# Kernel optimization log

Hardware: AMD Instinct MI355X
Metric: run time of the kernel (lower is better)

## Reference

```python
import jax, jax.numpy as jnp
import numpy as np
from jax import lax

LRELU_SLOPE = 0.2
GAIN = 2.0 ** 0.5
EPS = 1e-8


def setup_inputs() -> dict:
    key = jax.random.key(0)
    ks = jax.random.split(key, 8)
    B, NDW, CIN, COUT, H, W = 4, 512, 16, 16, 1024, 1024
    return {
        "w": jax.random.normal(ks[0], (B, NDW), jnp.float32),
        "x": jax.random.normal(ks[1], (B, CIN, H, W), jnp.float32),
        "noise": jax.random.normal(ks[2], (B, 1, H, W), jnp.float32),
        "fc_weight": jax.random.normal(ks[3], (CIN, NDW), jnp.float32),
        "fc_bias": jnp.ones((CIN,), jnp.float32),
        "conv_weight": jax.random.normal(ks[4], (COUT, CIN, 3, 3), jnp.float32),
        "conv_bias": jax.random.normal(ks[5], (COUT,), jnp.float32),
        "scale_noise": jnp.float32(0.1),
    }


def reference(w, x, noise, fc_weight, fc_bias, conv_weight, conv_bias, scale_noise):
    NDW = fc_weight.shape[1]
    COUT, CIN, KH, KW = conv_weight.shape
    # equal_lr scaling (FC): weight * n_dim_in**-0.5
    s = w @ (fc_weight.T * (NDW ** -0.5)) + fc_bias  # [B, CIN] style per input channel
    # equal_lr scaling (Conv): weight * (in_channels * k^2)**-0.5
    wc = conv_weight * ((CIN * KH * KW) ** -0.5)  # [COUT, CIN, 3, 3]
    # demodulation coefficient: d[b,o] = 1/sqrt(sum_{i,kh,kw} (s[b,i]*wc[o,i,kh,kw])^2 + eps)
    w2 = (wc ** 2).sum(axis=(2, 3))  # [COUT, CIN]
    d = lax.rsqrt((s ** 2) @ w2.T + EPS)  # [B, COUT]
    # modulate input instead of materializing per-sample weights (mathematically identical)
    xm = x * s[:, :, None, None]
    y = lax.conv_general_dilated(
        xm, wc, window_strides=(1, 1), padding=((1, 1), (1, 1)),
        dimension_numbers=("NCHW", "OIHW", "NCHW"))
    y = y * d[:, :, None, None] + conv_bias[None, :, None, None]
    y = y + scale_noise * noise  # broadcast noise over channels
    y = GAIN * jnp.where(y >= 0, y, LRELU_SLOPE * y)
    return (w, y)
```

## Files before the change

### kernel.cpp

```cpp
#include <hip/hip_runtime.h>

#define H_ 1024
#define W_ 1024
#define B_ 4
#define CIN 16
#define COUT 16
#define TH 8
#define TW 64
#define LDS_COLS 66
#define LDS_ROWS 10

#define LRELU 0.2f
#define GAIN_ 1.4142135623730951f
#define EPS_ 1e-8f

typedef __attribute__((ext_vector_type(8))) short bf16x8;
typedef __attribute__((ext_vector_type(4))) float f32x4;

static __device__ __forceinline__ unsigned short f32_to_bf16(float f) {
    unsigned int u = __float_as_uint(f);
    unsigned int r = u + 0x7FFF + ((u >> 16) & 1);
    return (unsigned short)(r >> 16);
}

__global__ __launch_bounds__(256) void k_setup1(
    const float* __restrict__ w, const float* __restrict__ fcw,
    const float* __restrict__ fcb, float* __restrict__ s_out,
    float* __restrict__ w_copy_out)
{
    __shared__ float part[256];
    const int tid = threadIdx.x;
    const int bi = tid >> 2;
    const int q  = tid & 3;
    const int b = bi >> 4, i = bi & 15;
    const float* wr = w + b * 512 + q * 128;
    const float* fr = fcw + i * 512 + q * 128;
    float acc = 0.f;
    #pragma unroll 8
    for (int k = 0; k < 128; ++k) acc += wr[k] * fr[k];
    part[tid] = acc;
    __syncthreads();
    if (tid < 64) {
        float v = part[tid*4] + part[tid*4+1] + part[tid*4+2] + part[tid*4+3];
        s_out[tid] = v * 0.04419417382415922f  + fcb[tid & 15];
    }
    for (int e = tid; e < B_ * 512; e += 256) w_copy_out[e] = w[e];
}

__global__ __launch_bounds__(256) void k_setup2(
    const float* __restrict__ s_in, const float* __restrict__ convw,
    unsigned short* __restrict__ afrag)
{
    const int b = blockIdx.x;
    const int tid = threadIdx.x;
    __shared__ float s_sh[16];
    __shared__ float d_sh[16];
    __shared__ float wc_sh[COUT * CIN * 9];
    __shared__ float part[256];

    if (tid < 16) s_sh[tid] = s_in[b * 16 + tid];
    for (int e = tid; e < COUT * CIN * 9; e += 256)
        wc_sh[e] = convw[e] * (1.0f / 12.0f);
    __syncthreads();

    const int o = tid >> 4, i = tid & 15;
    const float si = s_sh[i];
    float acc = 0.f;
    #pragma unroll
    for (int tap = 0; tap < 9; ++tap) {
        float v = wc_sh[(o * 16 + i) * 9 + tap] * si;
        acc += v * v;
    }
    part[tid] = acc;
    __syncthreads();
    if (tid < 16) {
        float sum = EPS_;
        #pragma unroll
        for (int j = 0; j < 16; ++j) sum += part[tid * 16 + j];
        d_sh[tid] = rsqrtf(sum);
    }
    __syncthreads();

    for (int e = tid; e < 5 * 64 * 8; e += 256) {
        int t = e >> 9;
        int lane = (e >> 3) & 63;
        int j = e & 7;
        int oo = lane & 15, g = lane >> 4;
        int ii = (g & 1) * 8 + j;
        int tap = 2 * t + (g >> 1);
        float v = 0.f;
        if (tap < 9) v = wc_sh[(oo * 16 + ii) * 9 + tap] * s_sh[ii] * d_sh[oo];
        afrag[(size_t)b * (5 * 64 * 8) + e] = f32_to_bf16(v);
    }
}

__global__ __launch_bounds__(256) void k_conv(
    const float* __restrict__ x, const float* __restrict__ noise,
    const float* __restrict__ conv_bias, const float* __restrict__ sn_ptr,
    const unsigned short* __restrict__ afrag, float* __restrict__ y)
{
    __shared__ unsigned short tile[2][LDS_ROWS][LDS_COLS][8];

    const int tid = threadIdx.x;
    const int bt = blockIdx.z;
    const int h0 = blockIdx.y * TH;
    const int w0 = blockIdx.x * TW;
    const float sn = sn_ptr[0];
    const float* xb = x + (size_t)bt * CIN * H_ * W_;

    if (tid < 160) {
        const int row = tid >> 4;
        const int cg  = tid & 15;
        const int gh  = h0 - 1 + row;
        const bool okr = (gh >= 0) && (gh < H_);
        #pragma unroll
        for (int h = 0; h < 2; ++h) {
            float4 v[8];
            #pragma unroll
            for (int c = 0; c < 8; ++c) {
                v[c] = make_float4(0.f, 0.f, 0.f, 0.f);
                if (okr)
                    v[c] = *reinterpret_cast<const float4*>(
                        xb + ((size_t)(8 * h + c) * H_ + gh) * W_ + (w0 + 4 * cg));
            }
            #pragma unroll
            for (int px = 0; px < 4; ++px) {
                bf16x8 pk;
                pk[0] = (short)f32_to_bf16(px == 0 ? v[0].x : px == 1 ? v[0].y : px == 2 ? v[0].z : v[0].w);
                pk[1] = (short)f32_to_bf16(px == 0 ? v[1].x : px == 1 ? v[1].y : px == 2 ? v[1].z : v[1].w);
                pk[2] = (short)f32_to_bf16(px == 0 ? v[2].x : px == 1 ? v[2].y : px == 2 ? v[2].z : v[2].w);
                pk[3] = (short)f32_to_bf16(px == 0 ? v[3].x : px == 1 ? v[3].y : px == 2 ? v[3].z : v[3].w);
                pk[4] = (short)f32_to_bf16(px == 0 ? v[4].x : px == 1 ? v[4].y : px == 2 ? v[4].z : v[4].w);
                pk[5] = (short)f32_to_bf16(px == 0 ? v[5].x : px == 1 ? v[5].y : px == 2 ? v[5].z : v[5].w);
                pk[6] = (short)f32_to_bf16(px == 0 ? v[6].x : px == 1 ? v[6].y : px == 2 ? v[6].z : v[6].w);
                pk[7] = (short)f32_to_bf16(px == 0 ? v[7].x : px == 1 ? v[7].y : px == 2 ? v[7].z : v[7].w);
                *reinterpret_cast<bf16x8*>(&tile[h][row][1 + 4 * cg + px][0]) = pk;
            }
        }
    } else if (tid < 180) {
        const int u    = tid - 160;
        const int row  = u >> 1;
        const int side = u & 1;
        const int col  = side * (LDS_COLS - 1);
        const int gh   = h0 - 1 + row;
        const int gw   = w0 - 1 + col;
        const bool ok  = (gh >= 0) && (gh < H_) && (gw >= 0) && (gw < W_);
        #pragma unroll
        for (int h = 0; h < 2; ++h) {
            bf16x8 pk;
            #pragma unroll
            for (int c = 0; c < 8; ++c) {
                float v = ok ? xb[((size_t)(8 * h + c) * H_ + gh) * W_ + gw] : 0.f;
                pk[c] = (short)f32_to_bf16(v);
            }
            *reinterpret_cast<bf16x8*>(&tile[h][row][col][0]) = pk;
        }
    }

    const int lane  = tid & 63;
    const int wid   = tid >> 6;
    const int p     = lane & 15;
    const int g     = lane >> 4;
    const int ghalf = g >> 1;
    const int chalf = g & 1;

    bf16x8 a[5];
    {
        const bf16x8* ap =
            reinterpret_cast<const bf16x8*>(afrag + (size_t)bt * 5 * 64 * 8);
        #pragma unroll
        for (int t = 0; t < 5; ++t) a[t] = ap[t * 64 + lane];
    }
    float bias_j[4];
    #pragma unroll
    for (int j = 0; j < 4; ++j) bias_j[j] = conv_bias[g * 4 + j];

    int lroff[5], lcoff[5];
    #pragma unroll
    for (int t = 0; t < 5; ++t) {
        int tap = 2 * t + ghalf;
        if (tap > 8) tap = 8;
        lroff[t] = tap / 3;
        lcoff[t] = tap % 3;
    }

    __syncthreads();

    float* yb = y + (size_t)bt * COUT * H_ * W_;
    const float* nb = noise + (size_t)bt * H_ * W_;

    #pragma unroll
    for (int rr = 0; rr < 2; ++rr) {
        const int oh = wid * 2 + rr;
        #pragma unroll
        for (int gc = 0; gc < 4; ++gc) {
            const int ow = gc * 16;
            f32x4 acc = {0.f, 0.f, 0.f, 0.f};
            #pragma unroll
            for (int t = 0; t < 5; ++t) {
                const bf16x8 bv = *reinterpret_cast<const bf16x8*>(
                    &tile[chalf][oh + lroff[t]][ow + p + lcoff[t]][0]);
                acc = __builtin_amdgcn_mfma_f32_16x16x32_bf16(a[t], bv, acc, 0, 0, 0);
            }
            const int gh = h0 + oh;
            const int gw = w0 + ow + p;
            const float noi = nb[(size_t)gh * W_ + gw] * sn;
            #pragma unroll
            for (int j = 0; j < 4; ++j) {
                float v = acc[j] + bias_j[j] + noi;
                v = (v >= 0.f) ? v : (LRELU * v);
                yb[((size_t)(g * 4 + j) * H_ + gh) * W_ + gw] = v * GAIN_;
            }
        }
    }
}

extern "C" void kernel_launch(void* const* d_in, const int* in_sizes, int n_in,
                              void* d_out, int out_size, void* d_ws, size_t ws_size,
                              hipStream_t stream)
{
    const float* w     = (const float*)d_in[0];
    const float* x     = (const float*)d_in[1];
    const float* noise = (const float*)d_in[2];
    const float* fcw   = (const float*)d_in[3];
    const float* fcb   = (const float*)d_in[4];
    const float* convw = (const float*)d_in[5];
    const float* convb = (const float*)d_in[6];
    const float* sn    = (const float*)d_in[7];

    float* out = (float*)d_out;
    float* ws_s = (float*)d_ws;
    unsigned short* ws_afrag = (unsigned short*)((char*)d_ws + 256);

    k_setup1<<<1, 256, 0, stream>>>(w, fcw, fcb, ws_s, out);
    k_setup2<<<B_, 256, 0, stream>>>(ws_s, convw, ws_afrag);
    dim3 grid(W_ / TW, H_ / TH, B_);
    k_conv<<<grid, 256, 0, stream>>>(x, noise, convb, sn, ws_afrag, out + 2048);
}
```

Measured before the change: 181.3 us.

## Loop each block over eight row tiles with double-buffered LDS staging

Each block now walks NT=8 consecutive 8-row tiles of a narrower 32-column strip. The global loads for the next tile are issued into registers before computing the current one and written to a second LDS buffer afterwards, so memory latency overlaps MFMA work. The padded LDS layout with a per-half column offset is meant to reduce bank conflicts, and the launch bound requests higher occupancy. In exchange the grid is much smaller and the narrower tile raises the halo overhead per column, so the vertical halo reloads per tile stay.

```diff
diff --git a/kernel.cpp b/kernel.cpp
--- a/kernel.cpp
+++ b/kernel.cpp
@@ -6,9 +6,11 @@
 #define CIN 16
 #define COUT 16
 #define TH 8
-#define TW 64
-#define LDS_COLS 66
-#define LDS_ROWS 10
+#define TW 32
+#define NT 8
+#define ROWS 10
+#define COLS 34
+#define COLS_P 36
 
 #define LRELU 0.2f
 #define GAIN_ 1.4142135623730951f
@@ -94,68 +96,21 @@
     }
 }
 
-__global__ __launch_bounds__(256) void k_conv(
+__global__ __launch_bounds__(256, 4) void k_conv(
     const float* __restrict__ x, const float* __restrict__ noise,
     const float* __restrict__ conv_bias, const float* __restrict__ sn_ptr,
     const unsigned short* __restrict__ afrag, float* __restrict__ y)
 {
-    __shared__ unsigned short tile[2][LDS_ROWS][LDS_COLS][8];
+    __shared__ unsigned short tile[2 * 2 * ROWS * COLS_P * 8];
 
     const int tid = threadIdx.x;
     const int bt = blockIdx.z;
-    const int h0 = blockIdx.y * TH;
+    const int h0 = blockIdx.y * (TH * NT);
     const int w0 = blockIdx.x * TW;
     const float sn = sn_ptr[0];
     const float* xb = x + (size_t)bt * CIN * H_ * W_;
-
-    if (tid < 160) {
-        const int row = tid >> 4;
-        const int cg  = tid & 15;
-        const int gh  = h0 - 1 + row;
-        const bool okr = (gh >= 0) && (gh < H_);
-        #pragma unroll
-        for (int h = 0; h < 2; ++h) {
-            float4 v[8];
-            #pragma unroll
-            for (int c = 0; c < 8; ++c) {
-                v[c] = make_float4(0.f, 0.f, 0.f, 0.f);
-                if (okr)
-                    v[c] = *reinterpret_cast<const float4*>(
-                        xb + ((size_t)(8 * h + c) * H_ + gh) * W_ + (w0 + 4 * cg));
-            }
-            #pragma unroll
-            for (int px = 0; px < 4; ++px) {
-                bf16x8 pk;
-                pk[0] = (short)f32_to_bf16(px == 0 ? v[0].x : px == 1 ? v[0].y : px == 2 ? v[0].z : v[0].w);
-                pk[1] = (short)f32_to_bf16(px == 0 ? v[1].x : px == 1 ? v[1].y : px == 2 ? v[1].z : v[1].w);
-                pk[2] = (short)f32_to_bf16(px == 0 ? v[2].x : px == 1 ? v[2].y : px == 2 ? v[2].z : v[2].w);
-                pk[3] = (short)f32_to_bf16(px == 0 ? v[3].x : px == 1 ? v[3].y : px == 2 ? v[3].z : v[3].w);
-                pk[4] = (short)f32_to_bf16(px == 0 ? v[4].x : px == 1 ? v[4].y : px == 2 ? v[4].z : v[4].w);
-                pk[5] = (short)f32_to_bf16(px == 0 ? v[5].x : px == 1 ? v[5].y : px == 2 ? v[5].z : v[5].w);
-                pk[6] = (short)f32_to_bf16(px == 0 ? v[6].x : px == 1 ? v[6].y : px == 2 ? v[6].z : v[6].w);
-                pk[7] = (short)f32_to_bf16(px == 0 ? v[7].x : px == 1 ? v[7].y : px == 2 ? v[7].z : v[7].w);
-                *reinterpret_cast<bf16x8*>(&tile[h][row][1 + 4 * cg + px][0]) = pk;
-            }
-        }
-    } else if (tid < 180) {
-        const int u    = tid - 160;
-        const int row  = u >> 1;
-        const int side = u & 1;
-        const int col  = side * (LDS_COLS - 1);
-        const int gh   = h0 - 1 + row;
-        const int gw   = w0 - 1 + col;
-        const bool ok  = (gh >= 0) && (gh < H_) && (gw >= 0) && (gw < W_);
-        #pragma unroll
-        for (int h = 0; h < 2; ++h) {
-            bf16x8 pk;
-            #pragma unroll
-            for (int c = 0; c < 8; ++c) {
-                float v = ok ? xb[((size_t)(8 * h + c) * H_ + gh) * W_ + gw] : 0.f;
-                pk[c] = (short)f32_to_bf16(v);
-            }
-            *reinterpret_cast<bf16x8*>(&tile[h][row][col][0]) = pk;
-        }
-    }
+    float* yb = y + (size_t)bt * COUT * H_ * W_;
+    const float* nb = noise + (size_t)bt * H_ * W_;
 
     const int lane  = tid & 63;
     const int wid   = tid >> 6;
@@ -164,10 +119,65 @@
     const int ghalf = g >> 1;
     const int chalf = g & 1;
 
+    const bool is_int  = (tid < 160);
+    const bool is_edge = (tid >= 160) && (tid < 200);
+    const int s_row = is_int ? (tid >> 4) : ((tid - 160) >> 2);
+    const int s_sub = tid & 15;
+    const int s_hh  = is_int ? (s_sub >> 3) : ((tid - 160) & 1);
+    const int s_cg  = s_sub & 7;
+    const int s_side = ((tid - 160) >> 1) & 1;
+
+    auto toff = [&](int buf, int half, int row, int col) -> int {
+        return (((buf * 2 + half) * ROWS + row) * COLS_P + col + 2 * half) * 8;
+    };
+
+    float4 v[8];
+    float  ev[8];
+
+    auto stage_load = [&](int t) {
+        const int gh0 = h0 + TH * t - 1;
+        if (is_int) {
+            const int gh = gh0 + s_row;
+            const bool ok = (gh >= 0) && (gh < H_);
+            const float* base = xb + ((size_t)(8 * s_hh) * H_ + gh) * W_ + (w0 + 4 * s_cg);
+            #pragma unroll
+            for (int c = 0; c < 8; ++c) {
+                v[c] = make_float4(0.f, 0.f, 0.f, 0.f);
+                if (ok) v[c] = *reinterpret_cast<const float4*>(base + (size_t)c * H_ * W_);
+            }
+        } else if (is_edge) {
+            const int gh = gh0 + s_row;
+            const int gw = w0 - 1 + s_side * (COLS - 1);
+            const bool ok = (gh >= 0) && (gh < H_) && (gw >= 0) && (gw < W_);
+            #pragma unroll
+            for (int c = 0; c < 8; ++c)
+                ev[c] = ok ? xb[((size_t)(8 * s_hh + c) * H_ + gh) * W_ + gw] : 0.f;
+        }
+    };
+
+    auto stage_write = [&](int buf) {
+        if (is_int) {
+            #pragma unroll
+            for (int px = 0; px < 4; ++px) {
+                bf16x8 pk;
+                #pragma unroll
+                for (int c = 0; c < 8; ++c) {
+                    float f = px == 0 ? v[c].x : px == 1 ? v[c].y : px == 2 ? v[c].z : v[c].w;
+                    pk[c] = (short)f32_to_bf16(f);
+                }
+                *reinterpret_cast<bf16x8*>(&tile[toff(buf, s_hh, s_row, 1 + 4 * s_cg + px)]) = pk;
+            }
+        } else if (is_edge) {
+            bf16x8 pk;
+            #pragma unroll
+            for (int c = 0; c < 8; ++c) pk[c] = (short)f32_to_bf16(ev[c]);
+            *reinterpret_cast<bf16x8*>(&tile[toff(buf, s_hh, s_row, s_side * (COLS - 1))]) = pk;
+        }
+    };
+
     bf16x8 a[5];
     {
-        const bf16x8* ap =
-            reinterpret_cast<const bf16x8*>(afrag + (size_t)bt * 5 * 64 * 8);
+        const bf16x8* ap = reinterpret_cast<const bf16x8*>(afrag + (size_t)bt * 5 * 64 * 8);
         #pragma unroll
         for (int t = 0; t < 5; ++t) a[t] = ap[t * 64 + lane];
     }
@@ -184,35 +194,43 @@
         lcoff[t] = tap % 3;
     }
 
-    __syncthreads();
-
-    float* yb = y + (size_t)bt * COUT * H_ * W_;
-    const float* nb = noise + (size_t)bt * H_ * W_;
-
-    #pragma unroll
-    for (int rr = 0; rr < 2; ++rr) {
-        const int oh = wid * 2 + rr;
+    auto compute = [&](int t, int buf) {
         #pragma unroll
-        for (int gc = 0; gc < 4; ++gc) {
-            const int ow = gc * 16;
-            f32x4 acc = {0.f, 0.f, 0.f, 0.f};
-            #pragma unroll
-            for (int t = 0; t < 5; ++t) {
-                const bf16x8 bv = *reinterpret_cast<const bf16x8*>(
-                    &tile[chalf][oh + lroff[t]][ow + p + lcoff[t]][0]);
-                acc = __builtin_amdgcn_mfma_f32_16x16x32_bf16(a[t], bv, acc, 0, 0, 0);
-            }
-            const int gh = h0 + oh;
-            const int gw = w0 + ow + p;
-            const float noi = nb[(size_t)gh * W_ + gw] * sn;
-            #pragma unroll
-            for (int j = 0; j < 4; ++j) {
-                float v = acc[j] + bias_j[j] + noi;
-                v = (v >= 0.f) ? v : (LRELU * v);
-                yb[((size_t)(g * 4 + j) * H_ + gh) * W_ + gw] = v * GAIN_;
+        for (int rr = 0; rr < 2; ++rr) {
+            const int oh = wid * 2 + rr;
+            #pragma unroll
+            for (int gc = 0; gc < 2; ++gc) {
+                const int ow = gc * 16;
+                f32x4 acc = {0.f, 0.f, 0.f, 0.f};
+                #pragma unroll
+                for (int tt = 0; tt < 5; ++tt) {
+                    const bf16x8 bv = *reinterpret_cast<const bf16x8*>(
+                        &tile[toff(buf, chalf, oh + lroff[tt], ow + p + lcoff[tt])]);
+                    acc = __builtin_amdgcn_mfma_f32_16x16x32_bf16(a[tt], bv, acc, 0, 0, 0);
+                }
+                const int gh = h0 + TH * t + oh;
+                const int gw = w0 + ow + p;
+                const float noi = nb[(size_t)gh * W_ + gw] * sn;
+                #pragma unroll
+                for (int j = 0; j < 4; ++j) {
+                    float vv = acc[j] + bias_j[j] + noi;
+                    vv = (vv >= 0.f) ? vv : (LRELU * vv);
+                    yb[((size_t)(g * 4 + j) * H_ + gh) * W_ + gw] = vv * GAIN_;
+                }
             }
         }
-    }
+    };
+
+    stage_load(0);
+    stage_write(0);
+    for (int t = 0; t < NT - 1; ++t) {
+        __syncthreads();
+        stage_load(t + 1);
+        compute(t, t & 1);
+        stage_write((t + 1) & 1);
+    }
+    __syncthreads();
+    compute(NT - 1, (NT - 1) & 1);
 }
 
 extern "C" void kernel_launch(void* const* d_in, const int* in_sizes, int n_in,
@@ -234,6 +252,6 @@
 
     k_setup1<<<1, 256, 0, stream>>>(w, fcw, fcb, ws_s, out);
     k_setup2<<<B_, 256, 0, stream>>>(ws_s, convw, ws_afrag);
-    dim3 grid(W_ / TW, H_ / TH, B_);
+    dim3 grid(W_ / TW, H_ / (TH * NT), B_);
     k_conv<<<grid, 256, 0, stream>>>(x, noise, convb, sn, ws_afrag, out + 2048);
 }
```

After: 272.6 us. +50.4%, slower.
